# Kernel tuning notes

Measured on AMD Instinct MI355X. Metric: run time of the kernel, lower is better.

Reference implementation:

```python
import jax, jax.numpy as jnp
import numpy as np

THRESHOLD = 0.9  # graph_threshold; graph_secondary is None
EPS = 1e-12


def setup_inputs() -> dict:
    key = jax.random.key(0)
    k_x, k_cw, k_cb, k_u, k_lw, k_lb = jax.random.split(key, 6)
    B = 8192
    x = jax.random.normal(k_x, (B, 1, 28, 28), dtype=jnp.float32)
    conv_w = jax.random.normal(k_cw, (4, 1, 2, 2), dtype=jnp.float32) * 0.5  # OIHW
    conv_b = jax.random.normal(k_cb, (4,), dtype=jnp.float32) * 0.1
    # random orthogonal 4x4 "quantum" unitary via QR, as in the torch buffer
    unitary = jnp.linalg.qr(jax.random.normal(k_u, (4, 4), dtype=jnp.float32))[0]
    D = 4 * 14 * 14  # conv_out * num_patches = 784
    lin_w = jax.random.normal(k_lw, (10, D), dtype=jnp.float32) * (1.0 / np.sqrt(D))
    lin_b = jax.random.normal(k_lb, (10,), dtype=jnp.float32) * 0.01
    return {"x": x, "conv_w": conv_w, "conv_b": conv_b, "unitary": unitary,
            "lin_w": lin_w, "lin_b": lin_b}


def _forward(x, conv_w, conv_b, unitary, lin_w, lin_b):
    B = x.shape[0]
    # _PatchConv: 2x2 conv, stride 2, then flatten to [B, 4*14*14]
    feats = jax.lax.conv_general_dilated(
        x, conv_w, window_strides=(2, 2), padding="VALID",
        dimension_numbers=("NCHW", "OIHW", "NCHW"))
    feats = feats + conv_b[None, :, None, None]
    flat = feats.reshape(B, -1)                      # [B, 784]
    # _QuantumPatchEncoder: reinterpret as [B, 196, 4], apply unitary^T
    patches = flat.reshape(B, -1, 4)
    qf = jnp.einsum("bnk,wk->bnw", patches, unitary).reshape(B, -1)  # [B, 784]
    # linear head + log_softmax
    logits = qf @ lin_w.T + lin_b
    log_probs = jax.nn.log_softmax(logits, axis=-1)
    # GraphAdjacencyLayer: pairwise squared-cosine fidelity, thresholded.
    # Vectorized: normalize rows, one GEMM, square, threshold.
    qn = qf / (jnp.linalg.norm(qf, axis=-1, keepdims=True) + EPS)   # [B, 784]
    fid = (qn @ qn.T) ** 2                                          # [B, B]
    adj = jnp.where(fid >= THRESHOLD, 1.0, 0.0).astype(jnp.float32)
    adj = adj * (1.0 - jnp.eye(B, dtype=jnp.float32))  # no self-edges (i<j pairs)
    return log_probs, adj


def reference(x, conv_w, conv_b, unitary, lin_w, lin_b):
    return _forward(x, conv_w, conv_b, unitary, lin_w, lin_b)
```

## Files before the change

### kernel.cpp

```cpp
#include <hip/hip_runtime.h>
#include <hip/hip_bf16.h>

typedef unsigned char uchar_t;
typedef __attribute__((ext_vector_type(4))) float f32x4;

#define B_SZ 8192
#define D_FT 784
#define K_PAD 832
#define N_KT 13
#define THRESH 0.9f

#define GLOBAL_AS(p) ((const __attribute__((address_space(1))) void*)(p))
#define LDS_AS(p)    ((__attribute__((address_space(3))) void*)(p))

__global__ __launch_bounds__(256) void zero_adj_kernel(float* __restrict__ adj)
{
    const size_t n4 = (size_t)B_SZ * B_SZ / 4;
    f32x4 z = {0.f, 0.f, 0.f, 0.f};
    f32x4* p = (f32x4*)adj;
    for (size_t i = (size_t)blockIdx.x * 256 + threadIdx.x; i < n4;
         i += (size_t)gridDim.x * 256)
        __builtin_nontemporal_store(z, p + i);
}

__global__ __launch_bounds__(256) void preproc_kernel(
    const float* __restrict__ x, const float* __restrict__ conv_w,
    const float* __restrict__ conv_b, const float* __restrict__ unitary,
    const float* __restrict__ lin_w, const float* __restrict__ lin_b,
    float* __restrict__ log_probs, uchar_t* __restrict__ qn)
{
    __shared__ float xr[4][784];
    __shared__ float qf[4][784];

    const int t = threadIdx.x, lane = t & 63, wave = t >> 6;
    const int b = blockIdx.x * 4 + wave;
    float* xw = xr[wave];
    float* qw = qf[wave];

    const float4* xsrc = (const float4*)(x + (size_t)b * 784);
    #pragma unroll
    for (int i = lane; i < 196; i += 64) ((float4*)xw)[i] = xsrc[i];
    __syncthreads();

    float sumsq = 0.f;
    for (int g = lane; g < 196; g += 64) {
        const int c = g / 49, p = g % 49;
        const float w00 = conv_w[c*4+0], w01 = conv_w[c*4+1];
        const float w10 = conv_w[c*4+2], w11 = conv_w[c*4+3];
        const float bcv = conv_b[c];
        float feat[4];
        #pragma unroll
        for (int j = 0; j < 4; ++j) {
            const int s = 4*p + j;
            const int h = s / 14, wq = s % 14;
            const float* px = &xw[(2*h)*28 + 2*wq];
            feat[j] = bcv + w00*px[0] + w01*px[1] + w10*px[28] + w11*px[29];
        }
        #pragma unroll
        for (int w = 0; w < 4; ++w) {
            float v = unitary[w*4+0]*feat[0] + unitary[w*4+1]*feat[1]
                    + unitary[w*4+2]*feat[2] + unitary[w*4+3]*feat[3];
            qw[4*g + w] = v;
            sumsq += v * v;
        }
    }
    __syncthreads();

    #pragma unroll
    for (int off = 1; off < 64; off <<= 1) sumsq += __shfl_xor(sumsq, off, 64);
    const float inv = 1.0f / (sqrtf(sumsq) + 1e-12f);

    unsigned int* qrow = (unsigned int*)(qn + (size_t)b * K_PAD);
    for (int i = lane; i < 208; i += 64) {
        unsigned int o = 0u;
        if (i < 196) {
            const float v0 = qw[4*i+0] * inv, v1 = qw[4*i+1] * inv;
            const float v2 = qw[4*i+2] * inv, v3 = qw[4*i+3] * inv;
            int lo = __builtin_amdgcn_cvt_pk_fp8_f32(v0, v1, 0, 0);
            o = (unsigned int)__builtin_amdgcn_cvt_pk_fp8_f32(v2, v3, lo, 1);
        }
        qrow[i] = o;
    }

    float acc[10];
    #pragma unroll
    for (int cl = 0; cl < 10; ++cl) acc[cl] = 0.f;
    for (int k = lane; k < 784; k += 64) {
        const float v = qw[k];
        #pragma unroll
        for (int cl = 0; cl < 10; ++cl) acc[cl] += v * lin_w[cl*784 + k];
    }
    #pragma unroll
    for (int cl = 0; cl < 10; ++cl) {
        #pragma unroll
        for (int off = 1; off < 64; off <<= 1)
            acc[cl] += __shfl_xor(acc[cl], off, 64);
        acc[cl] += lin_b[cl];
    }
    if (lane == 0) {
        float mx = -1e30f;
        #pragma unroll
        for (int cl = 0; cl < 10; ++cl) mx = fmaxf(mx, acc[cl]);
        float se = 0.f;
        #pragma unroll
        for (int cl = 0; cl < 10; ++cl) se += expf(acc[cl] - mx);
        const float lse = mx + logf(se);
        #pragma unroll
        for (int cl = 0; cl < 10; ++cl)
            log_probs[(size_t)b*10 + cl] = acc[cl] - lse;
    }
}

__global__ __launch_bounds__(256, 4) void gram_kernel(
    const uchar_t* __restrict__ qn, float* __restrict__ adj)
{
    const int t0 = blockIdx.x;
    int tl = (t0 & 7) * 260 + (t0 >> 3);
    int br = (int)((129.0 - sqrt(16641.0 - 8.0 * (double)tl)) * 0.5);
    while ((br + 1) * (129 - (br + 1)) / 2 <= tl) ++br;
    while (br * (129 - br) / 2 > tl) --br;
    const int bc = br + (tl - br * (129 - br) / 2);

    __shared__ uchar_t ldsA[2][8192] __attribute__((aligned(16)));
    __shared__ uchar_t ldsB[2][8192] __attribute__((aligned(16)));

    const int t = threadIdx.x;
    const int lane = t & 63, wave = t >> 6;
    const int wr = wave >> 1, wc = wave & 1;
    const int quad = lane >> 4, l16 = lane & 15;

    const int srow = lane & 15, sck = (lane >> 4) * 16;
    const uchar_t* gA0 = qn + (size_t)(br*128 + wave*16     + srow) * K_PAD + sck;
    const uchar_t* gA1 = qn + (size_t)(br*128 + (wave+4)*16 + srow) * K_PAD + sck;
    const uchar_t* gB0 = qn + (size_t)(bc*128 + wave*16     + srow) * K_PAD + sck;
    const uchar_t* gB1 = qn + (size_t)(bc*128 + (wave+4)*16 + srow) * K_PAD + sck;
    const int ld0 = wave * 1024, ld1 = (wave + 4) * 1024;

    #define STAGE(p, koff) do {                                                            \
        __builtin_amdgcn_global_load_lds(GLOBAL_AS(gA0 + (koff)), LDS_AS(&ldsA[p][ld0]), 16, 0, 0); \
        __builtin_amdgcn_global_load_lds(GLOBAL_AS(gA1 + (koff)), LDS_AS(&ldsA[p][ld1]), 16, 0, 0); \
        __builtin_amdgcn_global_load_lds(GLOBAL_AS(gB0 + (koff)), LDS_AS(&ldsB[p][ld0]), 16, 0, 0); \
        __builtin_amdgcn_global_load_lds(GLOBAL_AS(gB1 + (koff)), LDS_AS(&ldsB[p][ld1]), 16, 0, 0); \
    } while (0)

    f32x4 acc[4][4] = {};
    STAGE(0, 0);

    #pragma unroll
    for (int kt = 0; kt < N_KT; ++kt) {
        const int p = kt & 1;

        asm volatile("" ::: "memory");
        __builtin_amdgcn_s_waitcnt(0xF70);
        __builtin_amdgcn_s_barrier();
        asm volatile("" ::: "memory");

        if (kt + 1 < N_KT) STAGE(p ^ 1, (kt + 1) * 64);
        asm volatile("" ::: "memory");

        #pragma unroll
        for (int s = 0; s < 2; ++s) {
            const int fo = (2*s + (quad >> 1))*256 + l16*16 + (quad & 1)*8;
            long bfr[4];
            #pragma unroll
            for (int ni = 0; ni < 4; ++ni)
                bfr[ni] = *(const long*)&ldsB[p][(wc*4 + ni)*1024 + fo];
            #pragma unroll
            for (int mi = 0; mi < 4; ++mi) {
                const long af = *(const long*)&ldsA[p][(wr*4 + mi)*1024 + fo];
                #pragma unroll
                for (int ni = 0; ni < 4; ++ni)
                    acc[mi][ni] = __builtin_amdgcn_mfma_f32_16x16x32_fp8_fp8(
                        af, bfr[ni], acc[mi][ni], 0, 0, 0);
            }
        }
    }
    #undef STAGE

    const bool offdiag = (br != bc);
    #pragma unroll
    for (int mi = 0; mi < 4; ++mi) {
        const int gr0 = br*128 + wr*64 + mi*16 + quad*4;
        #pragma unroll
        for (int ni = 0; ni < 4; ++ni) {
            const int gc = bc*128 + wc*64 + ni*16 + l16;
            const f32x4 v = acc[mi][ni];
            float o[4];
            bool h = false;
            #pragma unroll
            for (int r = 0; r < 4; ++r) {
                o[r] = (v[r]*v[r] >= THRESH && (gr0 + r) != gc) ? 1.0f : 0.0f;
                h = h || (o[r] != 0.0f);
            }
            if (__any(h)) {
                #pragma unroll
                for (int r = 0; r < 4; ++r)
                    adj[(size_t)(gr0 + r) * B_SZ + gc] = o[r];
                if (offdiag)
                    *(float4*)&adj[(size_t)gc * B_SZ + gr0] =
                        make_float4(o[0], o[1], o[2], o[3]);
            }
        }
    }
}

extern "C" void kernel_launch(void* const* d_in, const int* in_sizes, int n_in,
                              void* d_out, int out_size, void* d_ws, size_t ws_size,
                              hipStream_t stream) {
    const float* x       = (const float*)d_in[0];
    const float* conv_w  = (const float*)d_in[1];
    const float* conv_b  = (const float*)d_in[2];
    const float* unitary = (const float*)d_in[3];
    const float* lin_w   = (const float*)d_in[4];
    const float* lin_b   = (const float*)d_in[5];

    float* log_probs = (float*)d_out;
    float* adj       = (float*)d_out + (size_t)B_SZ * 10;
    uchar_t* qn      = (uchar_t*)d_ws;

    zero_adj_kernel<<<4096, 256, 0, stream>>>(adj);
    preproc_kernel<<<B_SZ / 4, 256, 0, stream>>>(x, conv_w, conv_b, unitary,
                                                 lin_w, lin_b, log_probs, qn);
    gram_kernel<<<2080, 256, 0, stream>>>(qn, adj);
}
```

Before: 373.6 us.

## Fuse adjacency zero-fill into gram kernel main loop

Removes the separate zero-fill kernel and has each gram tile block zero its own 128x128 output tile (and its mirrored tile when off-diagonal) with nontemporal stores spread across the K loop iterations. The aim is to overlap the 256MB write traffic with the MFMA compute and drop a full-output pass plus a kernel launch. The vmcnt wait is relaxed to allow the outstanding zero stores, and a full wait plus barrier is added before the sparse 1.0 writes so they land after the zeros. Interleaving the stores adds memory pressure that may slow the fp8 GEMM pipeline.

```diff
diff --git a/kernel.cpp b/kernel.cpp
--- a/kernel.cpp
+++ b/kernel.cpp
@@ -12,16 +12,6 @@
 
 #define GLOBAL_AS(p) ((const __attribute__((address_space(1))) void*)(p))
 #define LDS_AS(p)    ((__attribute__((address_space(3))) void*)(p))
-
-__global__ __launch_bounds__(256) void zero_adj_kernel(float* __restrict__ adj)
-{
-    const size_t n4 = (size_t)B_SZ * B_SZ / 4;
-    f32x4 z = {0.f, 0.f, 0.f, 0.f};
-    f32x4* p = (f32x4*)adj;
-    for (size_t i = (size_t)blockIdx.x * 256 + threadIdx.x; i < n4;
-         i += (size_t)gridDim.x * 256)
-        __builtin_nontemporal_store(z, p + i);
-}
 
 __global__ __launch_bounds__(256) void preproc_kernel(
     const float* __restrict__ x, const float* __restrict__ conv_w,
@@ -129,6 +119,10 @@
     const int wr = wave >> 1, wc = wave & 1;
     const int quad = lane >> 4, l16 = lane & 15;
 
+    const bool offdiag = (br != bc);
+    const int br128 = br * 128, bc128 = bc * 128;
+    const int zmask = offdiag ? 8191 : 4095;
+
     const int srow = lane & 15, sck = (lane >> 4) * 16;
     const uchar_t* gA0 = qn + (size_t)(br*128 + wave*16     + srow) * K_PAD + sck;
     const uchar_t* gA1 = qn + (size_t)(br*128 + (wave+4)*16 + srow) * K_PAD + sck;
@@ -151,11 +145,30 @@
         const int p = kt & 1;
 
         asm volatile("" ::: "memory");
-        __builtin_amdgcn_s_waitcnt(0xF70);
+        if (kt == 0)
+            __builtin_amdgcn_s_waitcnt(0xF70);
+        else
+            __builtin_amdgcn_s_waitcnt(0xF73);
         __builtin_amdgcn_s_barrier();
         asm volatile("" ::: "memory");
 
         if (kt + 1 < N_KT) STAGE(p ^ 1, (kt + 1) * 64);
+        asm volatile("" ::: "memory");
+
+        {
+            f32x4 z = {0.f, 0.f, 0.f, 0.f};
+            #pragma unroll
+            for (int j = 0; j < 3; ++j) {
+                const int idx  = (kt * 768 + j * 256 + t) & zmask;
+                const int tile = idx >> 12;
+                const int r    = (idx >> 5) & 127;
+                const int c4   = idx & 31;
+                const int rowb = tile ? bc128 : br128;
+                const int colb = tile ? br128 : bc128;
+                __builtin_nontemporal_store(
+                    z, (f32x4*)adj + (size_t)(rowb + r) * 2048 + (colb >> 2) + c4);
+            }
+        }
         asm volatile("" ::: "memory");
 
         #pragma unroll
@@ -177,13 +190,17 @@
     }
     #undef STAGE
 
-    const bool offdiag = (br != bc);
+    asm volatile("" ::: "memory");
+    __builtin_amdgcn_s_waitcnt(0xF70);
+    __builtin_amdgcn_s_barrier();
+    asm volatile("" ::: "memory");
+
     #pragma unroll
     for (int mi = 0; mi < 4; ++mi) {
-        const int gr0 = br*128 + wr*64 + mi*16 + quad*4;
+        const int gr0 = br128 + wr*64 + mi*16 + quad*4;
         #pragma unroll
         for (int ni = 0; ni < 4; ++ni) {
-            const int gc = bc*128 + wc*64 + ni*16 + l16;
+            const int gc = bc128 + wc*64 + ni*16 + l16;
             const f32x4 v = acc[mi][ni];
             float o[4];
             bool h = false;
@@ -218,7 +235,6 @@
     float* adj       = (float*)d_out + (size_t)B_SZ * 10;
     uchar_t* qn      = (uchar_t*)d_ws;
 
-    zero_adj_kernel<<<4096, 256, 0, stream>>>(adj);
     preproc_kernel<<<B_SZ / 4, 256, 0, stream>>>(x, conv_w, conv_b, unitary,
                                                  lin_w, lin_b, log_probs, qn);
     gram_kernel<<<2080, 256, 0, stream>>>(qn, adj);
```

Measured after the change: 342.8 us. 8.2% less time.
